# Kernel tuning notes

Hardware: AMD Instinct MI355X
Metric: run time of the kernel (lower is better)

The kernel has to match this reference:

```python
import jax, jax.numpy as jnp
import numpy as np

N = 131072
IN, HID, OUT = 128, 256, 64
NUM_TASKS = 16
NUM_COPIES = 4
NUM_LAYERS = 3


def setup_inputs() -> dict:
    key = jax.random.key(0)
    ks = jax.random.split(key, 10)
    inputs = jax.random.normal(ks[0], (N, IN), dtype=jnp.float32)
    task_indices = jax.random.randint(ks[1], (N,), 0, NUM_TASKS, dtype=jnp.int32)
    copy_maps = jax.random.randint(ks[2], (NUM_LAYERS, NUM_TASKS), 0, NUM_COPIES, dtype=jnp.int32)
    # per-copy Linear weights, Kaiming-ish scale 1/sqrt(fan_in)
    W0 = jax.random.normal(ks[3], (NUM_COPIES, IN, HID), dtype=jnp.float32) / np.sqrt(IN)
    b0 = jax.random.normal(ks[4], (NUM_COPIES, HID), dtype=jnp.float32) * 0.01
    W1 = jax.random.normal(ks[5], (NUM_COPIES, HID, HID), dtype=jnp.float32) / np.sqrt(HID)
    b1 = jax.random.normal(ks[6], (NUM_COPIES, HID), dtype=jnp.float32) * 0.01
    W2 = jax.random.normal(ks[7], (NUM_COPIES, HID, OUT), dtype=jnp.float32) / np.sqrt(HID)
    b2 = jax.random.normal(ks[8], (NUM_COPIES, OUT), dtype=jnp.float32) * 0.01
    return {"inputs": inputs, "task_indices": task_indices, "copy_maps": copy_maps,
            "W0": W0, "b0": b0, "W1": W1, "b1": b1, "W2": W2, "b2": b2}


def _routed_layer(x, W, b, copy_idx, apply_tanh):
    # x: [N, d_in], W: [C, d_in, d_out], b: [C, d_out], copy_idx: [N]
    # Each token goes through exactly one copy's Linear. Equivalent to the
    # torch sort->per-copy-forward->unsort, expressed as masked accumulation
    # over the small fixed set of copies (avoids data-dependent shapes).
    y = jnp.zeros((x.shape[0], W.shape[2]), dtype=x.dtype)
    for c in range(W.shape[0]):
        mask = (copy_idx == c).astype(x.dtype)[:, None]  # [N, 1]
        y = y + mask * (x @ W[c] + b[c])
    return jnp.tanh(y) if apply_tanh else y


def reference(inputs, task_indices, copy_maps, W0, b0, W1, b1, W2, b2):
    x = inputs
    Ws = (W0, W1, W2)
    bs = (b0, b1, b2)
    for layer in range(NUM_LAYERS):
        copy_idx = copy_maps[layer][task_indices]  # [N] task->copy routing
        x = _routed_layer(x, Ws[layer], bs[layer], copy_idx,
                          apply_tanh=(layer != NUM_LAYERS - 1))
    return x
```

## Files before the change

### kernel.cpp

```cpp
#include <hip/hip_runtime.h>

#define N_TOK 131072
#define TILE 128
#define NT_MAX 1040

typedef __attribute__((ext_vector_type(8))) short s8v;
typedef __attribute__((ext_vector_type(4))) float f4v;
typedef unsigned short ushort_t;

__device__ __forceinline__ unsigned short f2bf(float x) {
    union { float f; unsigned u; } v; v.f = x;
    unsigned r = v.u + 0x7fffu + ((v.u >> 16) & 1u);
    return (unsigned short)(r >> 16);
}

__device__ __forceinline__ unsigned pk2(float a, float b) {
    union { float f; unsigned u; } x, y; x.f = a; y.f = b;
    return __byte_perm(x.u + 0x8000u, y.u + 0x8000u, 0x7632);
}

__device__ __forceinline__ float tanh_fast(float x) {
    float e = __builtin_amdgcn_exp2f(x * 2.8853900817779268f);
    float r = __builtin_amdgcn_rcpf(e + 1.0f);
    return __builtin_fmaf(-2.0f, r, 1.0f);
}

__global__ void prep_hist_kernel(const float* __restrict__ W0, const float* __restrict__ W1,
                                 const float* __restrict__ W2,
                                 ushort_t* __restrict__ W0p, ushort_t* __restrict__ W1p,
                                 ushort_t* __restrict__ W2p,
                                 const int* __restrict__ task, int* __restrict__ blockCounts) {
    if (blockIdx.x < 224) {
        int f = blockIdx.x * 256 + threadIdx.x;
        const float* src; ushort_t* dst; int K, N;
        if (f < 16384)      { src = W0; dst = W0p; K = 128; N = 256; }
        else if (f < 49152) { src = W1; dst = W1p; K = 256; N = 256; f -= 16384; }
        else                { src = W2; dst = W2p; K = 256; N = 64;  f -= 49152; }
        int fpc = (N >> 4) * (K >> 5) * 64;
        int c = f / fpc, r = f % fpc;
        int lane = r & 63;
        int kt = (r >> 6) % (K >> 5);
        int ftile = (r >> 6) / (K >> 5);
        int n = ftile * 16 + (lane & 15);
        int kbase = kt * 32 + (lane >> 4) * 8;
        const float* s = src + (size_t)c * K * N + (size_t)kbase * N + n;
        s8v pk;
#pragma unroll
        for (int j = 0; j < 8; j++) pk[j] = (short)f2bf(s[(size_t)j * N]);
        *reinterpret_cast<s8v*>(dst + ((size_t)(c * fpc + r) << 3)) = pk;
    } else {
        __shared__ int cnt[16];
        int t = threadIdx.x;
        int hb = blockIdx.x - 224;
        if (t < 16) cnt[t] = 0;
        __syncthreads();
        int base = hb * 2048 + t;
#pragma unroll
        for (int i = 0; i < 8; i++) atomicAdd(&cnt[task[base + i * 256]], 1);
        __syncthreads();
        if (t < 16) blockCounts[hb * 16 + t] = cnt[t];
    }
}

__global__ void sort_kernel(const int* __restrict__ task, const int* __restrict__ blockCounts,
                            int* __restrict__ tileTask, int* __restrict__ nT,
                            int* __restrict__ perm) {
    __shared__ int cntLds[1024];
    __shared__ int total[16], pref[16], rank[16];
    __shared__ int tokBase[16], tbase[17];
    int t = threadIdx.x, b = blockIdx.x;
    for (int i = t; i < 1024; i += 256) cntLds[i] = blockCounts[i];
    if (t < 16) rank[t] = 0;
    __syncthreads();
    if (t < 16) {
        int tot = 0, pf = 0;
#pragma unroll
        for (int bb = 0; bb < 64; bb++) {
            int v = cntLds[bb * 16 + t];
            tot += v;
            if (bb < b) pf += v;
        }
        total[t] = tot; pref[t] = pf;
    }
    __syncthreads();
    if (t == 0) {
        int tok = 0, tile = 0;
        for (int k = 0; k < 16; k++) {
            tokBase[k] = tok;
            tbase[k] = tile;
            int ntk = (total[k] + TILE - 1) / TILE;
            tok += ntk * TILE;
            tile += ntk;
        }
        tbase[16] = tile;
        if (b == 0) nT[0] = tile;
    }
    __syncthreads();
    if (b == 0) {
        for (int i = t; i < NT_MAX; i += 256) {
            int tk = 0;
            if (i < tbase[16]) {
#pragma unroll
                for (int k = 0; k < 16; k++) if (i >= tbase[k]) tk = k;
            }
            tileTask[i] = tk;
        }
        for (int i = t; i < 16 * TILE; i += 256) {
            int k = i >> 7, off = i & (TILE - 1);
            int idx = total[k] + off;
            int lim = ((total[k] + TILE - 1) / TILE) * TILE;
            if (idx < lim) perm[tokBase[k] + idx] = -1;
        }
    }
    int tk[8], my[8];
#pragma unroll
    for (int i = 0; i < 8; i++) {
        int idx = b * 2048 + i * 256 + t;
        tk[i] = task[idx];
        my[i] = atomicAdd(&rank[tk[i]], 1);
    }
#pragma unroll
    for (int i = 0; i < 8; i++) {
        int idx = b * 2048 + i * 256 + t;
        perm[tokBase[tk[i]] + pref[tk[i]] + my[i]] = idx;
    }
}

__launch_bounds__(512, 2)
__global__ void mlp_kernel(const float* __restrict__ x_in,
                           const int* __restrict__ cmap,
                           const float* __restrict__ b0,
                           const float* __restrict__ b1,
                           const float* __restrict__ b2,
                           const ushort_t* __restrict__ W0p,
                           const ushort_t* __restrict__ W1p,
                           const ushort_t* __restrict__ W2p,
                           const int* __restrict__ tileTask,
                           const int* __restrict__ nTp,
                           const int* __restrict__ perm,
                           float* __restrict__ out) {
    __shared__ __align__(16) ushort_t H1[32768];
    __shared__ __align__(16) ushort_t XH2[32768];

    int b = blockIdx.x;
    if (b >= nTp[0]) return;
    int t = threadIdx.x;
    int task = tileTask[b];
    int c0 = cmap[task], c1 = cmap[16 + task], c2 = cmap[32 + task];

    int w = t >> 6;
    int lane = t & 63;
    int l15 = lane & 15, lq = lane >> 4;
    int mt2 = w & 3, ntb2 = (w >> 2) * 4;

    const ushort_t* Wc0 = W0p + (size_t)c0 * 32768;
    const ushort_t* Wc1 = W1p + (size_t)c1 * 65536;
    const ushort_t* Wc2 = W2p + (size_t)c2 * 16384;

    {
        int r = t >> 2, q = t & 3;
        int tok = perm[b * TILE + r];
        float4 v[8];
#pragma unroll
        for (int j = 0; j < 8; j++) v[j] = make_float4(0.f, 0.f, 0.f, 0.f);
        if ((unsigned)tok < (unsigned)N_TOK) {
            const float4* src = reinterpret_cast<const float4*>(x_in) + (size_t)tok * 32 + q * 8;
#pragma unroll
            for (int j = 0; j < 8; j++) v[j] = src[j];
        }
        int fbase = ((r >> 4) * 4 + q) * 64;
#pragma unroll
        for (int gq = 0; gq < 4; gq++) {
            uint4 pk;
            pk.x = pk2(v[2 * gq].x, v[2 * gq].y);     pk.y = pk2(v[2 * gq].z, v[2 * gq].w);
            pk.z = pk2(v[2 * gq + 1].x, v[2 * gq + 1].y); pk.w = pk2(v[2 * gq + 1].z, v[2 * gq + 1].w);
            *reinterpret_cast<uint4*>(&XH2[(fbase + (r & 15) + 16 * gq) << 3]) = pk;
        }
    }
    __syncthreads();

    {
        f4v acc[2][8];
#pragma unroll
        for (int mi = 0; mi < 2; mi++) {
            f4v bv = *reinterpret_cast<const f4v*>(b0 + c0 * 256 + (2 * w + mi) * 16 + lq * 4);
#pragma unroll
            for (int nt = 0; nt < 8; nt++) acc[mi][nt] = bv;
        }
#pragma unroll
        for (int kt = 0; kt < 4; kt++) {
            s8v wa[2];
#pragma unroll
            for (int mi = 0; mi < 2; mi++)
                wa[mi] = *reinterpret_cast<const s8v*>(Wc0 + ((((2 * w + mi) * 4 + kt) * 64 + lane) << 3));
#pragma unroll
            for (int nt = 0; nt < 8; nt++) {
                s8v xb = *reinterpret_cast<const s8v*>(&XH2[((nt * 4 + kt) * 64 + lane) << 3]);
                acc[0][nt] = __builtin_amdgcn_mfma_f32_16x16x32_bf16(wa[0], xb, acc[0][nt], 0, 0, 0);
                acc[1][nt] = __builtin_amdgcn_mfma_f32_16x16x32_bf16(wa[1], xb, acc[1][nt], 0, 0, 0);
            }
        }
#pragma unroll
        for (int mi = 0; mi < 2; mi++) {
            int ft = 2 * w + mi;
            int kt_h = ft >> 1;
            int lanep = l15 + 16 * ((ft & 1) * 2 + (lq >> 1));
            int j0 = (lq & 1) * 4;
#pragma unroll
            for (int nt = 0; nt < 8; nt++) {
                float t0 = tanh_fast(acc[mi][nt][0]);
                float t1 = tanh_fast(acc[mi][nt][1]);
                float t2 = tanh_fast(acc[mi][nt][2]);
                float t3 = tanh_fast(acc[mi][nt][3]);
                uint2 pk; pk.x = pk2(t0, t1); pk.y = pk2(t2, t3);
                *reinterpret_cast<uint2*>(&H1[(((nt * 8 + kt_h) * 64 + lanep) << 3) + j0]) = pk;
            }
        }
    }
    __syncthreads();

    {
        f4v acc[2][8];
#pragma unroll
        for (int mi = 0; mi < 2; mi++) {
            f4v bv = *reinterpret_cast<const f4v*>(b1 + c1 * 256 + (2 * w + mi) * 16 + lq * 4);
#pragma unroll
            for (int nt = 0; nt < 8; nt++) acc[mi][nt] = bv;
        }
#pragma unroll
        for (int kt = 0; kt < 8; kt++) {
            s8v wa[2];
#pragma unroll
            for (int mi = 0; mi < 2; mi++)
                wa[mi] = *reinterpret_cast<const s8v*>(Wc1 + ((((2 * w + mi) * 8 + kt) * 64 + lane) << 3));
#pragma unroll
            for (int nt = 0; nt < 8; nt++) {
                s8v xb = *reinterpret_cast<const s8v*>(&H1[((nt * 8 + kt) * 64 + lane) << 3]);
                acc[0][nt] = __builtin_amdgcn_mfma_f32_16x16x32_bf16(wa[0], xb, acc[0][nt], 0, 0, 0);
                acc[1][nt] = __builtin_amdgcn_mfma_f32_16x16x32_bf16(wa[1], xb, acc[1][nt], 0, 0, 0);
            }
        }
#pragma unroll
        for (int mi = 0; mi < 2; mi++) {
            int ft = 2 * w + mi;
            int kt_h = ft >> 1;
            int lanep = l15 + 16 * ((ft & 1) * 2 + (lq >> 1));
            int j0 = (lq & 1) * 4;
#pragma unroll
            for (int nt = 0; nt < 8; nt++) {
                float t0 = tanh_fast(acc[mi][nt][0]);
                float t1 = tanh_fast(acc[mi][nt][1]);
                float t2 = tanh_fast(acc[mi][nt][2]);
                float t3 = tanh_fast(acc[mi][nt][3]);
                uint2 pk; pk.x = pk2(t0, t1); pk.y = pk2(t2, t3);
                *reinterpret_cast<uint2*>(&XH2[(((nt * 8 + kt_h) * 64 + lanep) << 3) + j0]) = pk;
            }
        }
    }
    __syncthreads();

    {
        f4v bv = *reinterpret_cast<const f4v*>(b2 + c2 * 64 + mt2 * 16 + lq * 4);
        f4v acc[4];
#pragma unroll
        for (int e = 0; e < 4; e++) acc[e] = bv;
#pragma unroll
        for (int kt = 0; kt < 8; kt++) {
            s8v wa = *reinterpret_cast<const s8v*>(Wc2 + (((mt2 * 8 + kt) * 64 + lane) << 3));
#pragma unroll
            for (int e = 0; e < 4; e++) {
                s8v xb = *reinterpret_cast<const s8v*>(&XH2[(((ntb2 + e) * 8 + kt) * 64 + lane) << 3]);
                acc[e] = __builtin_amdgcn_mfma_f32_16x16x32_bf16(wa, xb, acc[e], 0, 0, 0);
            }
        }
#pragma unroll
        for (int e = 0; e < 4; e++) {
            int tok = perm[b * TILE + (ntb2 + e) * 16 + l15];
            if ((unsigned)tok < (unsigned)N_TOK) {
                float4 o;
                o.x = acc[e][0]; o.y = acc[e][1]; o.z = acc[e][2]; o.w = acc[e][3];
                *reinterpret_cast<float4*>(out + (size_t)tok * 64 + mt2 * 16 + lq * 4) = o;
            }
        }
    }
}

extern "C" void kernel_launch(void* const* d_in, const int* in_sizes, int n_in,
                              void* d_out, int out_size, void* d_ws, size_t ws_size,
                              hipStream_t stream) {
    const float* inputs = (const float*)d_in[0];
    const int*   task   = (const int*)d_in[1];
    const int*   cmap   = (const int*)d_in[2];
    const float* W0     = (const float*)d_in[3];
    const float* b0     = (const float*)d_in[4];
    const float* W1     = (const float*)d_in[5];
    const float* b1     = (const float*)d_in[6];
    const float* W2     = (const float*)d_in[7];
    const float* b2     = (const float*)d_in[8];
    float* out = (float*)d_out;

    char* ws = (char*)d_ws;
    int* blockCounts = (int*)(ws + 0);
    int* nT          = (int*)(ws + 4096);
    int* tileTask    = (int*)(ws + 4160);
    int* perm        = (int*)(ws + 8320);
    ushort_t* W0p    = (ushort_t*)(ws + 540800);
    ushort_t* W1p    = (ushort_t*)(ws + 802944);
    ushort_t* W2p    = (ushort_t*)(ws + 1327232);

    prep_hist_kernel<<<288, 256, 0, stream>>>(W0, W1, W2, W0p, W1p, W2p, task, blockCounts);
    sort_kernel<<<64, 256, 0, stream>>>(task, blockCounts, tileTask, nT, perm);
    mlp_kernel<<<NT_MAX, 512, 0, stream>>>(inputs, cmap, b0, b1, b2,
                                           W0p, W1p, W2p, tileTask, nT, perm, out);
}
```

Measured before the change: 181.4 us.

## Make MLP kernel persistent per task with prefetch and 4x4 register tiling

Replaces the one-block-per-tile grid with 256 persistent blocks. Each block is assigned to one task and strides over that task's tiles, so copy indices and biases are loaded once per block. The input rows for the next tile are prefetched into registers while the current tile computes. Layers 0 and 1 switch to a 4x4 MFMA register tile per wave (4 feature groups x 2 token groups), which loads more operands per wave and raises register pressure. Load balance now depends on the per-task tile count, since each task gets only 16 blocks.

```diff
diff --git a/kernel.cpp b/kernel.cpp
--- a/kernel.cpp
+++ b/kernel.cpp
@@ -3,6 +3,7 @@
 #define N_TOK 131072
 #define TILE 128
 #define NT_MAX 1040
+#define NBLK 256
 
 typedef __attribute__((ext_vector_type(8))) short s8v;
 typedef __attribute__((ext_vector_type(4))) float f4v;
@@ -63,8 +64,7 @@
 }
 
 __global__ void sort_kernel(const int* __restrict__ task, const int* __restrict__ blockCounts,
-                            int* __restrict__ tileTask, int* __restrict__ nT,
-                            int* __restrict__ perm) {
+                            int* __restrict__ tbaseG, int* __restrict__ perm) {
     __shared__ int cntLds[1024];
     __shared__ int total[16], pref[16], rank[16];
     __shared__ int tokBase[16], tbase[17];
@@ -93,18 +93,10 @@
             tile += ntk;
         }
         tbase[16] = tile;
-        if (b == 0) nT[0] = tile;
     }
     __syncthreads();
     if (b == 0) {
-        for (int i = t; i < NT_MAX; i += 256) {
-            int tk = 0;
-            if (i < tbase[16]) {
-#pragma unroll
-                for (int k = 0; k < 16; k++) if (i >= tbase[k]) tk = k;
-            }
-            tileTask[i] = tk;
-        }
+        if (t < 17) tbaseG[t] = tbase[t];
         for (int i = t; i < 16 * TILE; i += 256) {
             int k = i >> 7, off = i & (TILE - 1);
             int idx = total[k] + off;
@@ -135,153 +127,191 @@
                            const ushort_t* __restrict__ W0p,
                            const ushort_t* __restrict__ W1p,
                            const ushort_t* __restrict__ W2p,
-                           const int* __restrict__ tileTask,
-                           const int* __restrict__ nTp,
+                           const int* __restrict__ tbaseG,
                            const int* __restrict__ perm,
                            float* __restrict__ out) {
     __shared__ __align__(16) ushort_t H1[32768];
     __shared__ __align__(16) ushort_t XH2[32768];
 
-    int b = blockIdx.x;
-    if (b >= nTp[0]) return;
+    int p = blockIdx.x;
+    int x = p & 7, s = p >> 3;
+    int k = 2 * x + (s >> 4), sub = s & 15;
+    int tBeg = tbaseG[k], tEnd = tbaseG[k + 1];
+    if (tBeg + sub >= tEnd) return;
+
     int t = threadIdx.x;
-    int task = tileTask[b];
-    int c0 = cmap[task], c1 = cmap[16 + task], c2 = cmap[32 + task];
+    int c0 = cmap[k], c1 = cmap[16 + k], c2 = cmap[32 + k];
 
     int w = t >> 6;
     int lane = t & 63;
     int l15 = lane & 15, lq = lane >> 4;
+    int fg = w & 3, tg = w >> 2;
     int mt2 = w & 3, ntb2 = (w >> 2) * 4;
 
     const ushort_t* Wc0 = W0p + (size_t)c0 * 32768;
     const ushort_t* Wc1 = W1p + (size_t)c1 * 65536;
     const ushort_t* Wc2 = W2p + (size_t)c2 * 16384;
 
+    f4v bv0[4], bv1[4], bv2;
+#pragma unroll
+    for (int mi = 0; mi < 4; mi++) {
+        bv0[mi] = *reinterpret_cast<const f4v*>(b0 + c0 * 256 + (4 * fg + mi) * 16 + lq * 4);
+        bv1[mi] = *reinterpret_cast<const f4v*>(b1 + c1 * 256 + (4 * fg + mi) * 16 + lq * 4);
+    }
+    bv2 = *reinterpret_cast<const f4v*>(b2 + c2 * 64 + mt2 * 16 + lq * 4);
+
+    int r = t >> 2, q = t & 3;
+    const float4* xbase = reinterpret_cast<const float4*>(x_in);
+    float4 v[8];
+#pragma unroll
+    for (int j = 0; j < 8; j++) v[j] = make_float4(0.f, 0.f, 0.f, 0.f);
+
+    int tile = tBeg + sub;
     {
-        int r = t >> 2, q = t & 3;
-        int tok = perm[b * TILE + r];
-        float4 v[8];
-#pragma unroll
-        for (int j = 0; j < 8; j++) v[j] = make_float4(0.f, 0.f, 0.f, 0.f);
-        if ((unsigned)tok < (unsigned)N_TOK) {
-            const float4* src = reinterpret_cast<const float4*>(x_in) + (size_t)tok * 32 + q * 8;
+        int ptok = perm[tile * TILE + r];
+        if ((unsigned)ptok < (unsigned)N_TOK) {
+            const float4* src = xbase + (size_t)ptok * 32 + q * 8;
 #pragma unroll
             for (int j = 0; j < 8; j++) v[j] = src[j];
         }
-        int fbase = ((r >> 4) * 4 + q) * 64;
-#pragma unroll
-        for (int gq = 0; gq < 4; gq++) {
-            uint4 pk;
-            pk.x = pk2(v[2 * gq].x, v[2 * gq].y);     pk.y = pk2(v[2 * gq].z, v[2 * gq].w);
-            pk.z = pk2(v[2 * gq + 1].x, v[2 * gq + 1].y); pk.w = pk2(v[2 * gq + 1].z, v[2 * gq + 1].w);
-            *reinterpret_cast<uint4*>(&XH2[(fbase + (r & 15) + 16 * gq) << 3]) = pk;
-        }
-    }
-    __syncthreads();
-
-    {
-        f4v acc[2][8];
-#pragma unroll
-        for (int mi = 0; mi < 2; mi++) {
-            f4v bv = *reinterpret_cast<const f4v*>(b0 + c0 * 256 + (2 * w + mi) * 16 + lq * 4);
-#pragma unroll
-            for (int nt = 0; nt < 8; nt++) acc[mi][nt] = bv;
-        }
-#pragma unroll
-        for (int kt = 0; kt < 4; kt++) {
-            s8v wa[2];
-#pragma unroll
-            for (int mi = 0; mi < 2; mi++)
-                wa[mi] = *reinterpret_cast<const s8v*>(Wc0 + ((((2 * w + mi) * 4 + kt) * 64 + lane) << 3));
-#pragma unroll
-            for (int nt = 0; nt < 8; nt++) {
-                s8v xb = *reinterpret_cast<const s8v*>(&XH2[((nt * 4 + kt) * 64 + lane) << 3]);
-                acc[0][nt] = __builtin_amdgcn_mfma_f32_16x16x32_bf16(wa[0], xb, acc[0][nt], 0, 0, 0);
-                acc[1][nt] = __builtin_amdgcn_mfma_f32_16x16x32_bf16(wa[1], xb, acc[1][nt], 0, 0, 0);
-            }
-        }
-#pragma unroll
-        for (int mi = 0; mi < 2; mi++) {
-            int ft = 2 * w + mi;
-            int kt_h = ft >> 1;
-            int lanep = l15 + 16 * ((ft & 1) * 2 + (lq >> 1));
-            int j0 = (lq & 1) * 4;
-#pragma unroll
-            for (int nt = 0; nt < 8; nt++) {
-                float t0 = tanh_fast(acc[mi][nt][0]);
-                float t1 = tanh_fast(acc[mi][nt][1]);
-                float t2 = tanh_fast(acc[mi][nt][2]);
-                float t3 = tanh_fast(acc[mi][nt][3]);
-                uint2 pk; pk.x = pk2(t0, t1); pk.y = pk2(t2, t3);
-                *reinterpret_cast<uint2*>(&H1[(((nt * 8 + kt_h) * 64 + lanep) << 3) + j0]) = pk;
-            }
-        }
-    }
-    __syncthreads();
-
-    {
-        f4v acc[2][8];
-#pragma unroll
-        for (int mi = 0; mi < 2; mi++) {
-            f4v bv = *reinterpret_cast<const f4v*>(b1 + c1 * 256 + (2 * w + mi) * 16 + lq * 4);
-#pragma unroll
-            for (int nt = 0; nt < 8; nt++) acc[mi][nt] = bv;
-        }
-#pragma unroll
-        for (int kt = 0; kt < 8; kt++) {
-            s8v wa[2];
-#pragma unroll
-            for (int mi = 0; mi < 2; mi++)
-                wa[mi] = *reinterpret_cast<const s8v*>(Wc1 + ((((2 * w + mi) * 8 + kt) * 64 + lane) << 3));
-#pragma unroll
-            for (int nt = 0; nt < 8; nt++) {
-                s8v xb = *reinterpret_cast<const s8v*>(&H1[((nt * 8 + kt) * 64 + lane) << 3]);
-                acc[0][nt] = __builtin_amdgcn_mfma_f32_16x16x32_bf16(wa[0], xb, acc[0][nt], 0, 0, 0);
-                acc[1][nt] = __builtin_amdgcn_mfma_f32_16x16x32_bf16(wa[1], xb, acc[1][nt], 0, 0, 0);
-            }
-        }
-#pragma unroll
-        for (int mi = 0; mi < 2; mi++) {
-            int ft = 2 * w + mi;
-            int kt_h = ft >> 1;
-            int lanep = l15 + 16 * ((ft & 1) * 2 + (lq >> 1));
-            int j0 = (lq & 1) * 4;
-#pragma unroll
-            for (int nt = 0; nt < 8; nt++) {
-                float t0 = tanh_fast(acc[mi][nt][0]);
-                float t1 = tanh_fast(acc[mi][nt][1]);
-                float t2 = tanh_fast(acc[mi][nt][2]);
-                float t3 = tanh_fast(acc[mi][nt][3]);
-                uint2 pk; pk.x = pk2(t0, t1); pk.y = pk2(t2, t3);
-                *reinterpret_cast<uint2*>(&XH2[(((nt * 8 + kt_h) * 64 + lanep) << 3) + j0]) = pk;
-            }
-        }
-    }
-    __syncthreads();
-
-    {
-        f4v bv = *reinterpret_cast<const f4v*>(b2 + c2 * 64 + mt2 * 16 + lq * 4);
-        f4v acc[4];
-#pragma unroll
-        for (int e = 0; e < 4; e++) acc[e] = bv;
-#pragma unroll
-        for (int kt = 0; kt < 8; kt++) {
-            s8v wa = *reinterpret_cast<const s8v*>(Wc2 + (((mt2 * 8 + kt) * 64 + lane) << 3));
+    }
+
+    for (; tile < tEnd; tile += 16) {
+        {
+            int fbase = ((r >> 4) * 4 + q) * 64;
+#pragma unroll
+            for (int gq = 0; gq < 4; gq++) {
+                uint4 pk;
+                pk.x = pk2(v[2 * gq].x, v[2 * gq].y);         pk.y = pk2(v[2 * gq].z, v[2 * gq].w);
+                pk.z = pk2(v[2 * gq + 1].x, v[2 * gq + 1].y); pk.w = pk2(v[2 * gq + 1].z, v[2 * gq + 1].w);
+                *reinterpret_cast<uint4*>(&XH2[(fbase + (r & 15) + 16 * gq) << 3]) = pk;
+            }
+        }
+        __syncthreads();
+
+        int ntile = tile + 16;
+        if (ntile < tEnd) {
+            int ptok = perm[ntile * TILE + r];
+            float4 a[8];
+#pragma unroll
+            for (int j = 0; j < 8; j++) a[j] = make_float4(0.f, 0.f, 0.f, 0.f);
+            if ((unsigned)ptok < (unsigned)N_TOK) {
+                const float4* src = xbase + (size_t)ptok * 32 + q * 8;
+#pragma unroll
+                for (int j = 0; j < 8; j++) a[j] = src[j];
+            }
+#pragma unroll
+            for (int j = 0; j < 8; j++) v[j] = a[j];
+        }
+
+        {
+            f4v acc[4][4];
+#pragma unroll
+            for (int mi = 0; mi < 4; mi++)
+#pragma unroll
+                for (int ni = 0; ni < 4; ni++)
+                    acc[mi][ni] = bv0[mi];
+#pragma unroll
+            for (int kt = 0; kt < 4; kt++) {
+                s8v wa[4], xb[4];
+#pragma unroll
+                for (int mi = 0; mi < 4; mi++)
+                    wa[mi] = *reinterpret_cast<const s8v*>(Wc0 + ((((4 * fg + mi) * 4 + kt) * 64 + lane) << 3));
+#pragma unroll
+                for (int ni = 0; ni < 4; ni++)
+                    xb[ni] = *reinterpret_cast<const s8v*>(&XH2[(((4 * tg + ni) * 4 + kt) * 64 + lane) << 3]);
+#pragma unroll
+                for (int mi = 0; mi < 4; mi++)
+#pragma unroll
+                    for (int ni = 0; ni < 4; ni++)
+                        acc[mi][ni] = __builtin_amdgcn_mfma_f32_16x16x32_bf16(wa[mi], xb[ni], acc[mi][ni], 0, 0, 0);
+            }
+#pragma unroll
+            for (int mi = 0; mi < 4; mi++) {
+                int ft = 4 * fg + mi;
+                int kt_h = ft >> 1;
+                int lanep = l15 + 16 * ((ft & 1) * 2 + (lq >> 1));
+                int j0 = (lq & 1) * 4;
+#pragma unroll
+                for (int ni = 0; ni < 4; ni++) {
+                    int nt = 4 * tg + ni;
+                    float t0 = tanh_fast(acc[mi][ni][0]);
+                    float t1 = tanh_fast(acc[mi][ni][1]);
+                    float t2 = tanh_fast(acc[mi][ni][2]);
+                    float t3 = tanh_fast(acc[mi][ni][3]);
+                    uint2 pk; pk.x = pk2(t0, t1); pk.y = pk2(t2, t3);
+                    *reinterpret_cast<uint2*>(&H1[(((nt * 8 + kt_h) * 64 + lanep) << 3) + j0]) = pk;
+                }
+            }
+        }
+        __syncthreads();
+
+        {
+            f4v acc[4][4];
+#pragma unroll
+            for (int mi = 0; mi < 4; mi++)
+#pragma unroll
+                for (int ni = 0; ni < 4; ni++)
+                    acc[mi][ni] = bv1[mi];
+#pragma unroll
+            for (int kt = 0; kt < 8; kt++) {
+                s8v wa[4], xb[4];
+#pragma unroll
+                for (int mi = 0; mi < 4; mi++)
+                    wa[mi] = *reinterpret_cast<const s8v*>(Wc1 + ((((4 * fg + mi) * 8 + kt) * 64 + lane) << 3));
+#pragma unroll
+                for (int ni = 0; ni < 4; ni++)
+                    xb[ni] = *reinterpret_cast<const s8v*>(&H1[(((4 * tg + ni) * 8 + kt) * 64 + lane) << 3]);
+#pragma unroll
+                for (int mi = 0; mi < 4; mi++)
+#pragma unroll
+                    for (int ni = 0; ni < 4; ni++)
+                        acc[mi][ni] = __builtin_amdgcn_mfma_f32_16x16x32_bf16(wa[mi], xb[ni], acc[mi][ni], 0, 0, 0);
+            }
+#pragma unroll
+            for (int mi = 0; mi < 4; mi++) {
+                int ft = 4 * fg + mi;
+                int kt_h = ft >> 1;
+                int lanep = l15 + 16 * ((ft & 1) * 2 + (lq >> 1));
+                int j0 = (lq & 1) * 4;
+#pragma unroll
+                for (int ni = 0; ni < 4; ni++) {
+                    int nt = 4 * tg + ni;
+                    float t0 = tanh_fast(acc[mi][ni][0]);
+                    float t1 = tanh_fast(acc[mi][ni][1]);
+                    float t2 = tanh_fast(acc[mi][ni][2]);
+                    float t3 = tanh_fast(acc[mi][ni][3]);
+                    uint2 pk; pk.x = pk2(t0, t1); pk.y = pk2(t2, t3);
+                    *reinterpret_cast<uint2*>(&XH2[(((nt * 8 + kt_h) * 64 + lanep) << 3) + j0]) = pk;
+                }
+            }
+        }
+        __syncthreads();
+
+        {
+            f4v acc2[4];
+#pragma unroll
+            for (int e = 0; e < 4; e++) acc2[e] = bv2;
+#pragma unroll
+            for (int kt = 0; kt < 8; kt++) {
+                s8v wa = *reinterpret_cast<const s8v*>(Wc2 + (((mt2 * 8 + kt) * 64 + lane) << 3));
+#pragma unroll
+                for (int e = 0; e < 4; e++) {
+                    s8v xb = *reinterpret_cast<const s8v*>(&XH2[(((ntb2 + e) * 8 + kt) * 64 + lane) << 3]);
+                    acc2[e] = __builtin_amdgcn_mfma_f32_16x16x32_bf16(wa, xb, acc2[e], 0, 0, 0);
+                }
+            }
 #pragma unroll
             for (int e = 0; e < 4; e++) {
-                s8v xb = *reinterpret_cast<const s8v*>(&XH2[(((ntb2 + e) * 8 + kt) * 64 + lane) << 3]);
-                acc[e] = __builtin_amdgcn_mfma_f32_16x16x32_bf16(wa, xb, acc[e], 0, 0, 0);
-            }
-        }
-#pragma unroll
-        for (int e = 0; e < 4; e++) {
-            int tok = perm[b * TILE + (ntb2 + e) * 16 + l15];
-            if ((unsigned)tok < (unsigned)N_TOK) {
-                float4 o;
-                o.x = acc[e][0]; o.y = acc[e][1]; o.z = acc[e][2]; o.w = acc[e][3];
-                *reinterpret_cast<float4*>(out + (size_t)tok * 64 + mt2 * 16 + lq * 4) = o;
-            }
-        }
+                int tok = perm[tile * TILE + (ntb2 + e) * 16 + l15];
+                if ((unsigned)tok < (unsigned)N_TOK) {
+                    float4 o;
+                    o.x = acc2[e][0]; o.y = acc2[e][1]; o.z = acc2[e][2]; o.w = acc2[e][3];
+                    *reinterpret_cast<float4*>(out + (size_t)tok * 64 + mt2 * 16 + lq * 4) = o;
+                }
+            }
+        }
+        __syncthreads();
     }
 }
 
@@ -301,15 +331,14 @@
 
     char* ws = (char*)d_ws;
     int* blockCounts = (int*)(ws + 0);
-    int* nT          = (int*)(ws + 4096);
-    int* tileTask    = (int*)(ws + 4160);
-    int* perm        = (int*)(ws + 8320);
-    ushort_t* W0p    = (ushort_t*)(ws + 540800);
-    ushort_t* W1p    = (ushort_t*)(ws + 802944);
-    ushort_t* W2p    = (ushort_t*)(ws + 1327232);
+    int* tbaseG      = (int*)(ws + 4096);
+    int* perm        = (int*)(ws + 4224);
+    ushort_t* W0p    = (ushort_t*)(ws + 536704);
+    ushort_t* W1p    = (ushort_t*)(ws + 798848);
+    ushort_t* W2p    = (ushort_t*)(ws + 1323136);
 
     prep_hist_kernel<<<288, 256, 0, stream>>>(W0, W1, W2, W0p, W1p, W2p, task, blockCounts);
-    sort_kernel<<<64, 256, 0, stream>>>(task, blockCounts, tileTask, nT, perm);
-    mlp_kernel<<<NT_MAX, 512, 0, stream>>>(inputs, cmap, b0, b1, b2,
-                                           W0p, W1p, W2p, tileTask, nT, perm, out);
-}
+    sort_kernel<<<64, 256, 0, stream>>>(task, blockCounts, tbaseG, perm);
+    mlp_kernel<<<NBLK, 512, 0, stream>>>(inputs, cmap, b0, b1, b2,
+                                         W0p, W1p, W2p, tbaseG, perm, out);
+}
```

Result: slower. 251.6 us (+38.7%).
